# Performance work log

Hardware: AMD Instinct MI355X
Metric: run time of the kernel (lower is better)

## Reference

```python
import jax, jax.numpy as jnp
import numpy as np

B, D, L = 4, 256, 4096

def setup_inputs() -> dict:
    key = jax.random.key(0)
    k1, k2, k3 = jax.random.split(key, 3)
    query = jax.random.normal(k1, (B, D, L), dtype=jnp.float32)
    context = jax.random.normal(k2, (B, D, L), dtype=jnp.float32)
    W_in = jax.random.normal(k3, (D, D), dtype=jnp.float32) * 0.02
    b_in = jnp.zeros((D,), dtype=jnp.float32)
    return {"query": query, "context": context, "W_in": W_in, "b_in": b_in}

def reference(query, context, W_in, b_in):
    # inputs are [B, D, L]; module transposes to [B, L, D]
    q = jnp.transpose(query, (0, 2, 1))    # [B, O, D]
    c = jnp.transpose(context, (0, 2, 1))  # [B, Q, D]
    # 'general': linear_in applied to query only (torch Linear: x @ W^T + b)
    q = q @ W_in.T + b_in
    # unscaled Luong attention: QK^T -> softmax -> A V
    scores = jnp.einsum('bod,bqd->boq', q, c)          # [B, O, Q]
    weights = jax.nn.softmax(scores, axis=-1)          # [B, O, Q]
    out = jnp.einsum('boq,bqd->bod', weights, c)       # [B, O, D]
    return (out, weights)
```

## Files before the change

kernel.cpp:

```cpp
#include <hip/hip_runtime.h>


#define BATCH 4
#define DDIM  256
#define LSEQ  4096
#define TQ    64

typedef float    f32x4 __attribute__((ext_vector_type(4)));
typedef _Float16 f16x8 __attribute__((ext_vector_type(8)));
typedef _Float16 f16x4 __attribute__((ext_vector_type(4)));

__device__ __forceinline__ void gld16(const void* g, void* l) {
  __builtin_amdgcn_global_load_lds((const __attribute__((address_space(1))) void*)g,
                                   (__attribute__((address_space(3))) void*)l, 16, 0, 0);
}

__global__ __launch_bounds__(256) void transpose_cast(
    const float* __restrict__ q_in, const float* __restrict__ c_in,
    _Float16* __restrict__ q_out, _Float16* __restrict__ c_out,
    _Float16* __restrict__ cD16)
{
  __shared__ float tile[64][68];
  const int which = blockIdx.z >> 2;
  const int b     = blockIdx.z & 3;
  const float* __restrict__ src = which ? c_in : q_in;
  _Float16* __restrict__ dst    = which ? c_out : q_out;
  const int l0 = blockIdx.x * 64, d0 = blockIdx.y * 64;
  const int tid = threadIdx.x;
  const int tr = tid >> 4, tc = (tid & 15) << 2;
#pragma unroll
  for (int i = 0; i < 4; ++i) {
    int d = tr + i * 16;
    f32x4 v = *(const f32x4*)(src + ((size_t)b * DDIM + d0 + d) * LSEQ + l0 + tc);
    *(f32x4*)&tile[d][tc] = v;
    if (which) {
      f16x4 h;
      h[0] = (_Float16)v[0]; h[1] = (_Float16)v[1];
      h[2] = (_Float16)v[2]; h[3] = (_Float16)v[3];
      *(f16x4*)(cD16 + ((size_t)b * DDIM + d0 + d) * LSEQ + l0 + tc) = h;
    }
  }
  __syncthreads();
#pragma unroll
  for (int i = 0; i < 4; ++i) {
    int l = tr + i * 16;
    f16x4 h;
    h[0] = (_Float16)tile[tc + 0][l];
    h[1] = (_Float16)tile[tc + 1][l];
    h[2] = (_Float16)tile[tc + 2][l];
    h[3] = (_Float16)tile[tc + 3][l];
    *(f16x4*)(dst + ((size_t)b * LSEQ + l0 + l) * DDIM + d0 + tc) = h;
  }
}

__global__ __launch_bounds__(256) void wconv(const float* __restrict__ w,
                                             _Float16* __restrict__ w16) {
  int i = (blockIdx.x * 256 + threadIdx.x) * 4;
  f32x4 v = *(const f32x4*)(w + i);
  f16x4 h;
  h[0] = (_Float16)v[0]; h[1] = (_Float16)v[1];
  h[2] = (_Float16)v[2]; h[3] = (_Float16)v[3];
  *(f16x4*)(w16 + i) = h;
}

__global__ __launch_bounds__(256) void linear_q(
    const _Float16* __restrict__ qT16, const _Float16* __restrict__ W16,
    const float* __restrict__ bias, _Float16* __restrict__ qw16)
{
  const int tid = threadIdx.x;
  const int wv = tid >> 6, ln = tid & 63, g = ln >> 4, c16 = ln & 15;
  const size_t r0 = (size_t)blockIdx.x * 64 + wv * 16;

  f16x8 qa[8];
  const _Float16* qrow = qT16 + (r0 + c16) * DDIM + g * 8;
#pragma unroll
  for (int kk = 0; kk < 8; ++kk) qa[kk] = *(const f16x8*)(qrow + kk * 32);

  f32x4 acc[16];
#pragma unroll
  for (int n = 0; n < 16; ++n) acc[n] = f32x4{0.f, 0.f, 0.f, 0.f};

#pragma unroll 2
  for (int kk = 0; kk < 8; ++kk) {
#pragma unroll
    for (int n = 0; n < 16; ++n) {
      f16x8 bf = *(const f16x8*)(W16 + (n * 16 + c16) * DDIM + kk * 32 + g * 8);
      acc[n] = __builtin_amdgcn_mfma_f32_16x16x32_f16(qa[kk], bf, acc[n], 0, 0, 0);
    }
  }
#pragma unroll
  for (int n = 0; n < 16; ++n) {
    float bb = bias[n * 16 + c16];
#pragma unroll
    for (int r = 0; r < 4; ++r)
      qw16[(r0 + 4 * g + r) * DDIM + n * 16 + c16] = (_Float16)(acc[n][r] + bb);
  }
}

__global__ __launch_bounds__(1024, 4) void attn_main(
    const _Float16* __restrict__ qw16,
    const _Float16* __restrict__ cT16,
    const _Float16* __restrict__ cD16,
    float* __restrict__ outp,
    float* __restrict__ wgt)
{
  __shared__ __align__(16) char smem[2][32768];
  __shared__ __align__(16) char wbuf[8192];
  __shared__ float redbuf[4][64];
  char* obuf = &smem[0][0];

  const int tid = threadIdx.x;
  const int wv  = tid >> 6;
  const int qw  = wv & 3;
  const int ow  = wv >> 2;
  const int kh  = wv & 1;
  const int dw  = wv >> 1;
  const int ln  = tid & 63;
  const int g   = ln >> 4;
  const int c16 = ln & 15;

  const int lin   = blockIdx.y * 64 + blockIdx.x;
  const int b     = (lin & 7) >> 1;
  const int otile = ((lin >> 3) << 1) | (lin & 1);
  const int o0    = otile * 64;
  const int bo    = b * LSEQ + o0;

  const _Float16* __restrict__ cbase = cT16 + (size_t)b * LSEQ * DDIM;
  const _Float16* __restrict__ cDb   = cD16 + (size_t)b * DDIM * LSEQ;

  f16x8 qb[8];
#pragma unroll
  for (int kk = 0; kk < 8; ++kk)
    qb[kk] = *(const f16x8*)(qw16 +
        ((size_t)(bo + ow * 16 + c16) << 8) + kk * 32 + g * 8);

  auto issue_dma = [&](int t, int pp) {
#pragma unroll
    for (int i = 0; i < 2; ++i) {
      unsigned x  = (unsigned)tid * 16 + i * 16384;
      unsigned q  = x >> 9;
      unsigned db = (x & 511u) ^ ((q & 7u) << 4);
      gld16(cbase + ((size_t)(t * TQ + q) << 8) + (db >> 1), &smem[pp][x]);
    }
  };

  float lsum = 0.f;
  int p = 0;
  issue_dma(0, 0);
  for (int t = 0; t < LSEQ / TQ; ++t) {
    asm volatile("s_waitcnt vmcnt(0)" ::: "memory");
    __builtin_amdgcn_s_barrier();
    issue_dma(t < LSEQ / TQ - 1 ? t + 1 : 0, p ^ 1);
    __builtin_amdgcn_sched_barrier(0);

    const char* cl = smem[p];
    f32x4 sa{0.f, 0.f, 0.f, 0.f};
#pragma unroll
    for (int kk = 0; kk < 8; ++kk) {
      unsigned off = (unsigned)((qw * 16 + c16) * 512 + kk * 64 + g * 16) ^
                     ((unsigned)(c16 & 7) << 4);
      f16x8 af = *(const f16x8*)(cl + off);
      sa = __builtin_amdgcn_mfma_f32_16x16x32_f16(af, qb[kk], sa, 0, 0, 0);
    }
#pragma unroll
    for (int r = 0; r < 4; ++r) lsum += __expf(sa[r]);
    p ^= 1;
  }

  lsum += __shfl_xor(lsum, 16);
  lsum += __shfl_xor(lsum, 32);
  if (ln < 16) redbuf[qw][ow * 16 + ln] = lsum;
  __syncthreads();
  const int o_mine = ow * 16 + c16;
  const float invl = 1.0f / (redbuf[0][o_mine] + redbuf[1][o_mine] +
                             redbuf[2][o_mine] + redbuf[3][o_mine]);

  f32x4 oacc[4][2];
#pragma unroll
  for (int m = 0; m < 4; ++m)
#pragma unroll
    for (int nf = 0; nf < 2; ++nf) oacc[m][nf] = f32x4{0.f, 0.f, 0.f, 0.f};

  for (int t = 0; t < LSEQ / TQ; ++t) {
    const int q0 = t * TQ;
    if (t == 0) asm volatile("s_waitcnt vmcnt(0)" ::: "memory");
    else        asm volatile("s_waitcnt vmcnt(1)" ::: "memory");
    __builtin_amdgcn_s_barrier();
    __builtin_amdgcn_sched_barrier(0);

    f16x8 bv[2];
#pragma unroll
    for (int nf = 0; nf < 2; ++nf)
      bv[nf] = *(const f16x8*)(cDb +
          ((size_t)(dw * 32 + nf * 16 + c16) << 12) + q0 + kh * 32 + g * 8);

    if (t < LSEQ / TQ - 1) issue_dma(t + 1, p ^ 1);

    const char* cl = smem[p];
    f32x4 sa{0.f, 0.f, 0.f, 0.f};
#pragma unroll
    for (int kk = 0; kk < 8; ++kk) {
      unsigned off = (unsigned)((qw * 16 + c16) * 512 + kk * 64 + g * 16) ^
                     ((unsigned)(c16 & 7) << 4);
      f16x8 af = *(const f16x8*)(cl + off);
      sa = __builtin_amdgcn_mfma_f32_16x16x32_f16(af, qb[kk], sa, 0, 0, 0);
    }

    {
      f32x4 wv4;
      f16x4 wh;
#pragma unroll
      for (int r = 0; r < 4; ++r) {
        float w = __expf(sa[r]) * invl;
        wv4[r] = w;
        wh[r]  = (_Float16)w;
      }
      *(f32x4*)(wgt + ((size_t)(bo + o_mine) << 12) + q0 + qw * 16 + 4 * g) = wv4;
      unsigned wb = (unsigned)(o_mine * 128 + (qw * 16 + 4 * g) * 2) ^
                    ((unsigned)(o_mine & 7) << 4);
      *(f16x4*)(wbuf + wb) = wh;
    }
    asm volatile("s_waitcnt lgkmcnt(0)" ::: "memory");
    __builtin_amdgcn_s_barrier();
    __builtin_amdgcn_sched_barrier(0);

#pragma unroll
    for (int m = 0; m < 4; ++m) {
      unsigned off = (unsigned)((m * 16 + c16) * 128 + kh * 64 + g * 16) ^
                     ((unsigned)(c16 & 7) << 4);
      f16x8 wa = *(const f16x8*)(wbuf + off);
#pragma unroll
      for (int nf = 0; nf < 2; ++nf)
        oacc[m][nf] =
            __builtin_amdgcn_mfma_f32_16x16x32_f16(wa, bv[nf], oacc[m][nf], 0, 0, 0);
    }
    p ^= 1;
  }

  __syncthreads();
  if (kh == 1) {
#pragma unroll
    for (int m = 0; m < 4; ++m)
#pragma unroll
      for (int nf = 0; nf < 2; ++nf)
        *(f32x4*)(obuf + dw * 8192 + (m * 2 + nf) * 1024 + ln * 16) = oacc[m][nf];
  }
  __syncthreads();
  if (kh == 0) {
#pragma unroll
    for (int m = 0; m < 4; ++m)
#pragma unroll
      for (int nf = 0; nf < 2; ++nf) {
        f32x4 o2 = *(const f32x4*)(obuf + dw * 8192 + (m * 2 + nf) * 1024 + ln * 16);
        f32x4 o  = oacc[m][nf] + o2;
#pragma unroll
        for (int r = 0; r < 4; ++r)
          outp[((size_t)(bo + m * 16 + 4 * g + r) << 8) + dw * 32 + nf * 16 + c16] = o[r];
      }
  }
}

extern "C" void kernel_launch(void* const* d_in, const int* in_sizes, int n_in,
                              void* d_out, int out_size, void* d_ws, size_t ws_size,
                              hipStream_t stream) {
  const float* query   = (const float*)d_in[0];
  const float* context = (const float*)d_in[1];
  const float* W_in    = (const float*)d_in[2];
  const float* b_in    = (const float*)d_in[3];

  float* outp = (float*)d_out;
  float* wgt  = outp + (size_t)BATCH * LSEQ * DDIM;

  const size_t NELEM = (size_t)BATCH * LSEQ * DDIM;
  _Float16* qT16 = (_Float16*)d_ws;
  _Float16* cT16 = qT16 + NELEM;
  _Float16* qw16 = cT16 + NELEM;
  _Float16* W16  = qw16 + NELEM;
  _Float16* cD16 = W16 + 65536;

  transpose_cast<<<dim3(LSEQ / 64, DDIM / 64, 2 * BATCH), 256, 0, stream>>>(
      query, context, qT16, cT16, cD16);
  wconv<<<(DDIM * DDIM) / 1024, 256, 0, stream>>>(W_in, W16);
  linear_q<<<(BATCH * LSEQ) / 64, 256, 0, stream>>>(qT16, W16, b_in, qw16);
  attn_main<<<dim3(64, BATCH), 1024, 0, stream>>>(qw16, cT16, cD16, outp, wgt);
}
```

Measured before the change: 266.7 us.

## Double query tile per iteration and remap waves to reuse LDS context fragments

Raises the per-iteration context tile from 64 to 128 rows, doubling the LDS double buffers and the weight staging buffer. Each wave now computes scores for two 16-row output fragments against one context fragment, so every LDS read of context feeds two MFMAs, and the barrier count per pass is halved. The cost is 144KB+ of LDS and more registers, which forces one block per CU (launch bounds lowered to 1) and gives less latency hiding across blocks.

```diff
diff --git a/kernel.cpp b/kernel.cpp
--- a/kernel.cpp
+++ b/kernel.cpp
@@ -4,7 +4,7 @@
 #define BATCH 4
 #define DDIM  256
 #define LSEQ  4096
-#define TQ    64
+#define TQ    128
 
 typedef float    f32x4 __attribute__((ext_vector_type(4)));
 typedef _Float16 f16x8 __attribute__((ext_vector_type(8)));
@@ -97,24 +97,24 @@
   }
 }
 
-__global__ __launch_bounds__(1024, 4) void attn_main(
+__global__ __launch_bounds__(1024, 1) void attn_main(
     const _Float16* __restrict__ qw16,
     const _Float16* __restrict__ cT16,
     const _Float16* __restrict__ cD16,
     float* __restrict__ outp,
     float* __restrict__ wgt)
 {
-  __shared__ __align__(16) char smem[2][32768];
-  __shared__ __align__(16) char wbuf[8192];
-  __shared__ float redbuf[4][64];
+  __shared__ __align__(16) char smem[2][65536];
+  __shared__ __align__(16) char wbuf[16384];
+  __shared__ float redbuf[8][64];
   char* obuf = &smem[0][0];
 
   const int tid = threadIdx.x;
   const int wv  = tid >> 6;
-  const int qw  = wv & 3;
-  const int ow  = wv >> 2;
+  const int qs  = wv >> 1;
+  const int os  = wv & 1;
+  const int dw  = wv >> 1;
   const int kh  = wv & 1;
-  const int dw  = wv >> 1;
   const int ln  = tid & 63;
   const int g   = ln >> 4;
   const int c16 = ln & 15;
@@ -128,15 +128,17 @@
   const _Float16* __restrict__ cbase = cT16 + (size_t)b * LSEQ * DDIM;
   const _Float16* __restrict__ cDb   = cD16 + (size_t)b * DDIM * LSEQ;
 
-  f16x8 qb[8];
-#pragma unroll
-  for (int kk = 0; kk < 8; ++kk)
-    qb[kk] = *(const f16x8*)(qw16 +
-        ((size_t)(bo + ow * 16 + c16) << 8) + kk * 32 + g * 8);
+  f16x8 qb[2][8];
+#pragma unroll
+  for (int of = 0; of < 2; ++of)
+#pragma unroll
+    for (int kk = 0; kk < 8; ++kk)
+      qb[of][kk] = *(const f16x8*)(qw16 +
+          ((size_t)(bo + os * 32 + of * 16 + c16) << 8) + kk * 32 + g * 8);
 
   auto issue_dma = [&](int t, int pp) {
 #pragma unroll
-    for (int i = 0; i < 2; ++i) {
+    for (int i = 0; i < 4; ++i) {
       unsigned x  = (unsigned)tid * 16 + i * 16384;
       unsigned q  = x >> 9;
       unsigned db = (x & 511u) ^ ((q & 7u) << 4);
@@ -144,7 +146,20 @@
     }
   };
 
-  float lsum = 0.f;
+  auto scores = [&](const char* cl, f32x4& sa0, f32x4& sa1) {
+    sa0 = f32x4{0.f, 0.f, 0.f, 0.f};
+    sa1 = f32x4{0.f, 0.f, 0.f, 0.f};
+#pragma unroll
+    for (int kk = 0; kk < 8; ++kk) {
+      unsigned off = (unsigned)((qs * 16 + c16) * 512 + kk * 64 + g * 16) ^
+                     ((unsigned)(c16 & 7) << 4);
+      f16x8 af = *(const f16x8*)(cl + off);
+      sa0 = __builtin_amdgcn_mfma_f32_16x16x32_f16(af, qb[0][kk], sa0, 0, 0, 0);
+      sa1 = __builtin_amdgcn_mfma_f32_16x16x32_f16(af, qb[1][kk], sa1, 0, 0, 0);
+    }
+  };
+
+  float lsum0 = 0.f, lsum1 = 0.f;
   int p = 0;
   issue_dma(0, 0);
   for (int t = 0; t < LSEQ / TQ; ++t) {
@@ -153,27 +168,32 @@
     issue_dma(t < LSEQ / TQ - 1 ? t + 1 : 0, p ^ 1);
     __builtin_amdgcn_sched_barrier(0);
 
-    const char* cl = smem[p];
-    f32x4 sa{0.f, 0.f, 0.f, 0.f};
-#pragma unroll
-    for (int kk = 0; kk < 8; ++kk) {
-      unsigned off = (unsigned)((qw * 16 + c16) * 512 + kk * 64 + g * 16) ^
-                     ((unsigned)(c16 & 7) << 4);
-      f16x8 af = *(const f16x8*)(cl + off);
-      sa = __builtin_amdgcn_mfma_f32_16x16x32_f16(af, qb[kk], sa, 0, 0, 0);
-    }
-#pragma unroll
-    for (int r = 0; r < 4; ++r) lsum += __expf(sa[r]);
+    f32x4 sa0, sa1;
+    scores(smem[p], sa0, sa1);
+#pragma unroll
+    for (int r = 0; r < 4; ++r) {
+      lsum0 += __expf(sa0[r]);
+      lsum1 += __expf(sa1[r]);
+    }
     p ^= 1;
   }
 
-  lsum += __shfl_xor(lsum, 16);
-  lsum += __shfl_xor(lsum, 32);
-  if (ln < 16) redbuf[qw][ow * 16 + ln] = lsum;
+  lsum0 += __shfl_xor(lsum0, 16); lsum0 += __shfl_xor(lsum0, 32);
+  lsum1 += __shfl_xor(lsum1, 16); lsum1 += __shfl_xor(lsum1, 32);
+  if (ln < 16) {
+    redbuf[qs][os * 32 + ln]      = lsum0;
+    redbuf[qs][os * 32 + 16 + ln] = lsum1;
+  }
   __syncthreads();
-  const int o_mine = ow * 16 + c16;
-  const float invl = 1.0f / (redbuf[0][o_mine] + redbuf[1][o_mine] +
-                             redbuf[2][o_mine] + redbuf[3][o_mine]);
+  float invl[2];
+#pragma unroll
+  for (int of = 0; of < 2; ++of) {
+    int o = os * 32 + of * 16 + c16;
+    float s = 0.f;
+#pragma unroll
+    for (int k = 0; k < 8; ++k) s += redbuf[k][o];
+    invl[of] = 1.0f / s;
+  }
 
   f32x4 oacc[4][2];
 #pragma unroll
@@ -184,40 +204,39 @@
   for (int t = 0; t < LSEQ / TQ; ++t) {
     const int q0 = t * TQ;
     if (t == 0) asm volatile("s_waitcnt vmcnt(0)" ::: "memory");
-    else        asm volatile("s_waitcnt vmcnt(1)" ::: "memory");
+    else        asm volatile("s_waitcnt vmcnt(2)" ::: "memory");
     __builtin_amdgcn_s_barrier();
     __builtin_amdgcn_sched_barrier(0);
 
-    f16x8 bv[2];
+    f16x8 bv[2][2];
 #pragma unroll
     for (int nf = 0; nf < 2; ++nf)
-      bv[nf] = *(const f16x8*)(cDb +
-          ((size_t)(dw * 32 + nf * 16 + c16) << 12) + q0 + kh * 32 + g * 8);
+#pragma unroll
+      for (int ks = 0; ks < 2; ++ks)
+        bv[nf][ks] = *(const f16x8*)(cDb +
+            ((size_t)(dw * 32 + nf * 16 + c16) << 12) +
+            q0 + kh * 64 + ks * 32 + g * 8);
 
     if (t < LSEQ / TQ - 1) issue_dma(t + 1, p ^ 1);
 
-    const char* cl = smem[p];
-    f32x4 sa{0.f, 0.f, 0.f, 0.f};
-#pragma unroll
-    for (int kk = 0; kk < 8; ++kk) {
-      unsigned off = (unsigned)((qw * 16 + c16) * 512 + kk * 64 + g * 16) ^
-                     ((unsigned)(c16 & 7) << 4);
-      f16x8 af = *(const f16x8*)(cl + off);
-      sa = __builtin_amdgcn_mfma_f32_16x16x32_f16(af, qb[kk], sa, 0, 0, 0);
-    }
-
-    {
+    f32x4 sa0, sa1;
+    scores(smem[p], sa0, sa1);
+
+#pragma unroll
+    for (int of = 0; of < 2; ++of) {
+      f32x4 sv = of ? sa1 : sa0;
       f32x4 wv4;
       f16x4 wh;
 #pragma unroll
       for (int r = 0; r < 4; ++r) {
-        float w = __expf(sa[r]) * invl;
+        float w = __expf(sv[r]) * invl[of];
         wv4[r] = w;
         wh[r]  = (_Float16)w;
       }
-      *(f32x4*)(wgt + ((size_t)(bo + o_mine) << 12) + q0 + qw * 16 + 4 * g) = wv4;
-      unsigned wb = (unsigned)(o_mine * 128 + (qw * 16 + 4 * g) * 2) ^
-                    ((unsigned)(o_mine & 7) << 4);
+      int o = os * 32 + of * 16 + c16;
+      *(f32x4*)(wgt + ((size_t)(bo + o) << 12) + q0 + qs * 16 + 4 * g) = wv4;
+      unsigned wb = (unsigned)(o * 256 + (qs * 16 + 4 * g) * 2) ^
+                    ((unsigned)(o & 7) << 4);
       *(f16x4*)(wbuf + wb) = wh;
     }
     asm volatile("s_waitcnt lgkmcnt(0)" ::: "memory");
@@ -225,14 +244,17 @@
     __builtin_amdgcn_sched_barrier(0);
 
 #pragma unroll
-    for (int m = 0; m < 4; ++m) {
-      unsigned off = (unsigned)((m * 16 + c16) * 128 + kh * 64 + g * 16) ^
-                     ((unsigned)(c16 & 7) << 4);
-      f16x8 wa = *(const f16x8*)(wbuf + off);
-#pragma unroll
-      for (int nf = 0; nf < 2; ++nf)
-        oacc[m][nf] =
-            __builtin_amdgcn_mfma_f32_16x16x32_f16(wa, bv[nf], oacc[m][nf], 0, 0, 0);
+    for (int ks = 0; ks < 2; ++ks) {
+#pragma unroll
+      for (int m = 0; m < 4; ++m) {
+        unsigned off = (unsigned)((m * 16 + c16) * 256 + kh * 128 + ks * 64 + g * 16) ^
+                       ((unsigned)(c16 & 7) << 4);
+        f16x8 wa = *(const f16x8*)(wbuf + off);
+#pragma unroll
+        for (int nf = 0; nf < 2; ++nf)
+          oacc[m][nf] =
+              __builtin_amdgcn_mfma_f32_16x16x32_f16(wa, bv[nf][ks], oacc[m][nf], 0, 0, 0);
+      }
     }
     p ^= 1;
   }
```

Result: slower. 389.0 us (+45.9%).

## Halve attention block to 32 query rows with 512 threads, doubling grid

Applied to the files above, without the earlier changes.

Each attention block now handles 32 query rows with 8 waves instead of 64 rows with 16 waves, and the grid doubles to 512 blocks. Warp roles are remapped so each wave covers 64 output columns with 4 MFMA n-fragments, and context DMA uses 4 loads per thread. Score computation is factored into a lambda and moved ahead of the value loads. This raises block count for better CU load balance, but each block still streams the full context, so total context traffic from L2/LDS doubles.

```diff
diff --git a/kernel.cpp b/kernel.cpp
--- a/kernel.cpp
+++ b/kernel.cpp
@@ -97,7 +97,7 @@
   }
 }
 
-__global__ __launch_bounds__(1024, 4) void attn_main(
+__global__ __launch_bounds__(512, 4) void attn_main(
     const _Float16* __restrict__ qw16,
     const _Float16* __restrict__ cT16,
     const _Float16* __restrict__ cD16,
@@ -105,16 +105,16 @@
     float* __restrict__ wgt)
 {
   __shared__ __align__(16) char smem[2][32768];
-  __shared__ __align__(16) char wbuf[8192];
-  __shared__ float redbuf[4][64];
+  __shared__ __align__(16) char wbuf[4096];
+  __shared__ float redbuf[4][32];
   char* obuf = &smem[0][0];
 
   const int tid = threadIdx.x;
   const int wv  = tid >> 6;
-  const int qw  = wv & 3;
-  const int ow  = wv >> 2;
+  const int qs  = wv >> 1;
+  const int os  = wv & 1;
+  const int dw  = wv >> 1;
   const int kh  = wv & 1;
-  const int dw  = wv >> 1;
   const int ln  = tid & 63;
   const int g   = ln >> 4;
   const int c16 = ln & 15;
@@ -122,7 +122,7 @@
   const int lin   = blockIdx.y * 64 + blockIdx.x;
   const int b     = (lin & 7) >> 1;
   const int otile = ((lin >> 3) << 1) | (lin & 1);
-  const int o0    = otile * 64;
+  const int o0    = otile * 32;
   const int bo    = b * LSEQ + o0;
 
   const _Float16* __restrict__ cbase = cT16 + (size_t)b * LSEQ * DDIM;
@@ -132,19 +132,31 @@
 #pragma unroll
   for (int kk = 0; kk < 8; ++kk)
     qb[kk] = *(const f16x8*)(qw16 +
-        ((size_t)(bo + ow * 16 + c16) << 8) + kk * 32 + g * 8);
+        ((size_t)(bo + os * 16 + c16) << 8) + kk * 32 + g * 8);
 
   auto issue_dma = [&](int t, int pp) {
 #pragma unroll
-    for (int i = 0; i < 2; ++i) {
-      unsigned x  = (unsigned)tid * 16 + i * 16384;
+    for (int i = 0; i < 4; ++i) {
+      unsigned x  = (unsigned)tid * 16 + i * 8192;
       unsigned q  = x >> 9;
       unsigned db = (x & 511u) ^ ((q & 7u) << 4);
       gld16(cbase + ((size_t)(t * TQ + q) << 8) + (db >> 1), &smem[pp][x]);
     }
   };
 
-  float lsum = 0.f;
+  auto scores = [&](const char* cl) {
+    f32x4 sa{0.f, 0.f, 0.f, 0.f};
+#pragma unroll
+    for (int kk = 0; kk < 8; ++kk) {
+      unsigned off = (unsigned)((qs * 16 + c16) * 512 + kk * 64 + g * 16) ^
+                     ((unsigned)(c16 & 7) << 4);
+      f16x8 af = *(const f16x8*)(cl + off);
+      sa = __builtin_amdgcn_mfma_f32_16x16x32_f16(af, qb[kk], sa, 0, 0, 0);
+    }
+    return sa;
+  };
+
+  float ls = 0.f;
   int p = 0;
   issue_dma(0, 0);
   for (int t = 0; t < LSEQ / TQ; ++t) {
@@ -153,33 +165,25 @@
     issue_dma(t < LSEQ / TQ - 1 ? t + 1 : 0, p ^ 1);
     __builtin_amdgcn_sched_barrier(0);
 
-    const char* cl = smem[p];
-    f32x4 sa{0.f, 0.f, 0.f, 0.f};
-#pragma unroll
-    for (int kk = 0; kk < 8; ++kk) {
-      unsigned off = (unsigned)((qw * 16 + c16) * 512 + kk * 64 + g * 16) ^
-                     ((unsigned)(c16 & 7) << 4);
-      f16x8 af = *(const f16x8*)(cl + off);
-      sa = __builtin_amdgcn_mfma_f32_16x16x32_f16(af, qb[kk], sa, 0, 0, 0);
-    }
-#pragma unroll
-    for (int r = 0; r < 4; ++r) lsum += __expf(sa[r]);
+    f32x4 sa = scores(smem[p]);
+#pragma unroll
+    for (int r = 0; r < 4; ++r) ls += __expf(sa[r]);
     p ^= 1;
   }
 
-  lsum += __shfl_xor(lsum, 16);
-  lsum += __shfl_xor(lsum, 32);
-  if (ln < 16) redbuf[qw][ow * 16 + ln] = lsum;
-  __syncthreads();
-  const int o_mine = ow * 16 + c16;
+  ls += __shfl_xor(ls, 16);
+  ls += __shfl_xor(ls, 32);
+  if (ln < 16) redbuf[qs][os * 16 + ln] = ls;
+  __syncthreads();
+  const int o_mine = os * 16 + c16;
   const float invl = 1.0f / (redbuf[0][o_mine] + redbuf[1][o_mine] +
                              redbuf[2][o_mine] + redbuf[3][o_mine]);
 
-  f32x4 oacc[4][2];
-#pragma unroll
-  for (int m = 0; m < 4; ++m)
-#pragma unroll
-    for (int nf = 0; nf < 2; ++nf) oacc[m][nf] = f32x4{0.f, 0.f, 0.f, 0.f};
+  f32x4 oacc[2][4];
+#pragma unroll
+  for (int m = 0; m < 2; ++m)
+#pragma unroll
+    for (int nf = 0; nf < 4; ++nf) oacc[m][nf] = f32x4{0.f, 0.f, 0.f, 0.f};
 
   for (int t = 0; t < LSEQ / TQ; ++t) {
     const int q0 = t * TQ;
@@ -188,23 +192,15 @@
     __builtin_amdgcn_s_barrier();
     __builtin_amdgcn_sched_barrier(0);
 
-    f16x8 bv[2];
-#pragma unroll
-    for (int nf = 0; nf < 2; ++nf)
+    if (t < LSEQ / TQ - 1) issue_dma(t + 1, p ^ 1);
+
+    f32x4 sa = scores(smem[p]);
+
+    f16x8 bv[4];
+#pragma unroll
+    for (int nf = 0; nf < 4; ++nf)
       bv[nf] = *(const f16x8*)(cDb +
-          ((size_t)(dw * 32 + nf * 16 + c16) << 12) + q0 + kh * 32 + g * 8);
-
-    if (t < LSEQ / TQ - 1) issue_dma(t + 1, p ^ 1);
-
-    const char* cl = smem[p];
-    f32x4 sa{0.f, 0.f, 0.f, 0.f};
-#pragma unroll
-    for (int kk = 0; kk < 8; ++kk) {
-      unsigned off = (unsigned)((qw * 16 + c16) * 512 + kk * 64 + g * 16) ^
-                     ((unsigned)(c16 & 7) << 4);
-      f16x8 af = *(const f16x8*)(cl + off);
-      sa = __builtin_amdgcn_mfma_f32_16x16x32_f16(af, qb[kk], sa, 0, 0, 0);
-    }
+          ((size_t)(dw * 64 + nf * 16 + c16) << 12) + q0 + kh * 32 + g * 8);
 
     {
       f32x4 wv4;
@@ -215,8 +211,8 @@
         wv4[r] = w;
         wh[r]  = (_Float16)w;
       }
-      *(f32x4*)(wgt + ((size_t)(bo + o_mine) << 12) + q0 + qw * 16 + 4 * g) = wv4;
-      unsigned wb = (unsigned)(o_mine * 128 + (qw * 16 + 4 * g) * 2) ^
+      *(f32x4*)(wgt + ((size_t)(bo + o_mine) << 12) + q0 + qs * 16 + 4 * g) = wv4;
+      unsigned wb = (unsigned)(o_mine * 128 + (qs * 16 + 4 * g) * 2) ^
                     ((unsigned)(o_mine & 7) << 4);
       *(f16x4*)(wbuf + wb) = wh;
     }
@@ -225,12 +221,12 @@
     __builtin_amdgcn_sched_barrier(0);
 
 #pragma unroll
-    for (int m = 0; m < 4; ++m) {
+    for (int m = 0; m < 2; ++m) {
       unsigned off = (unsigned)((m * 16 + c16) * 128 + kh * 64 + g * 16) ^
                      ((unsigned)(c16 & 7) << 4);
       f16x8 wa = *(const f16x8*)(wbuf + off);
 #pragma unroll
-      for (int nf = 0; nf < 2; ++nf)
+      for (int nf = 0; nf < 4; ++nf)
         oacc[m][nf] =
             __builtin_amdgcn_mfma_f32_16x16x32_f16(wa, bv[nf], oacc[m][nf], 0, 0, 0);
     }
@@ -240,22 +236,22 @@
   __syncthreads();
   if (kh == 1) {
 #pragma unroll
-    for (int m = 0; m < 4; ++m)
-#pragma unroll
-      for (int nf = 0; nf < 2; ++nf)
-        *(f32x4*)(obuf + dw * 8192 + (m * 2 + nf) * 1024 + ln * 16) = oacc[m][nf];
+    for (int m = 0; m < 2; ++m)
+#pragma unroll
+      for (int nf = 0; nf < 4; ++nf)
+        *(f32x4*)(obuf + dw * 8192 + (m * 4 + nf) * 1024 + ln * 16) = oacc[m][nf];
   }
   __syncthreads();
   if (kh == 0) {
 #pragma unroll
-    for (int m = 0; m < 4; ++m)
-#pragma unroll
-      for (int nf = 0; nf < 2; ++nf) {
-        f32x4 o2 = *(const f32x4*)(obuf + dw * 8192 + (m * 2 + nf) * 1024 + ln * 16);
+    for (int m = 0; m < 2; ++m)
+#pragma unroll
+      for (int nf = 0; nf < 4; ++nf) {
+        f32x4 o2 = *(const f32x4*)(obuf + dw * 8192 + (m * 4 + nf) * 1024 + ln * 16);
         f32x4 o  = oacc[m][nf] + o2;
 #pragma unroll
         for (int r = 0; r < 4; ++r)
-          outp[((size_t)(bo + m * 16 + 4 * g + r) << 8) + dw * 32 + nf * 16 + c16] = o[r];
+          outp[((size_t)(bo + m * 16 + 4 * g + r) << 8) + dw * 64 + nf * 16 + c16] = o[r];
       }
   }
 }
@@ -282,5 +278,5 @@
       query, context, qT16, cT16, cD16);
   wconv<<<(DDIM * DDIM) / 1024, 256, 0, stream>>>(W_in, W16);
   linear_q<<<(BATCH * LSEQ) / 64, 256, 0, stream>>>(qT16, W16, b_in, qw16);
-  attn_main<<<dim3(64, BATCH), 1024, 0, stream>>>(qw16, cT16, cD16, outp, wgt);
-}
+  attn_main<<<dim3(64, 8), 512, 0, stream>>>(qw16, cT16, cD16, outp, wgt);
+}
```

Result: slower. 310.7 us (+16.5%).

## Software-pipeline second pass: compute next tile's scores alongside current PV MFMAs

Applied to the files above, without the earlier changes.

Restructures the second pass into a prologue, steady state and epilogue so the QK^T scores for tile t+1 are computed in the same iteration as the weights-times-context MFMAs for tile t. The DMA prefetch now runs two tiles ahead. The exp/normalize/store of the weights happens after a barrier, so the PV and score MFMAs can interleave and one barrier wait per tile is hidden. The risk is higher register pressure and subtle ordering hazards on the shared wbuf and smem buffers.

```diff
diff --git a/kernel.cpp b/kernel.cpp
--- a/kernel.cpp
+++ b/kernel.cpp
@@ -144,7 +144,36 @@
     }
   };
 
-  float lsum = 0.f;
+  auto scores = [&](const char* cl) {
+    f32x4 sa{0.f, 0.f, 0.f, 0.f};
+#pragma unroll
+    for (int kk = 0; kk < 8; ++kk) {
+      unsigned off = (unsigned)((qw * 16 + c16) * 512 + kk * 64 + g * 16) ^
+                     ((unsigned)(c16 & 7) << 4);
+      f16x8 af = *(const f16x8*)(cl + off);
+      sa = __builtin_amdgcn_mfma_f32_16x16x32_f16(af, qb[kk], sa, 0, 0, 0);
+    }
+    return sa;
+  };
+
+  const int o_mine = ow * 16 + c16;
+
+  auto emit_w = [&](const f32x4& sa, int q0, float invl) {
+    f32x4 wv4;
+    f16x4 wh;
+#pragma unroll
+    for (int r = 0; r < 4; ++r) {
+      float w = __expf(sa[r]) * invl;
+      wv4[r] = w;
+      wh[r]  = (_Float16)w;
+    }
+    *(f32x4*)(wgt + ((size_t)(bo + o_mine) << 12) + q0 + qw * 16 + 4 * g) = wv4;
+    unsigned wb = (unsigned)(o_mine * 128 + (qw * 16 + 4 * g) * 2) ^
+                  ((unsigned)(o_mine & 7) << 4);
+    *(f16x4*)(wbuf + wb) = wh;
+  };
+
+  float ls = 0.f;
   int p = 0;
   issue_dma(0, 0);
   for (int t = 0; t < LSEQ / TQ; ++t) {
@@ -153,25 +182,16 @@
     issue_dma(t < LSEQ / TQ - 1 ? t + 1 : 0, p ^ 1);
     __builtin_amdgcn_sched_barrier(0);
 
-    const char* cl = smem[p];
-    f32x4 sa{0.f, 0.f, 0.f, 0.f};
-#pragma unroll
-    for (int kk = 0; kk < 8; ++kk) {
-      unsigned off = (unsigned)((qw * 16 + c16) * 512 + kk * 64 + g * 16) ^
-                     ((unsigned)(c16 & 7) << 4);
-      f16x8 af = *(const f16x8*)(cl + off);
-      sa = __builtin_amdgcn_mfma_f32_16x16x32_f16(af, qb[kk], sa, 0, 0, 0);
-    }
-#pragma unroll
-    for (int r = 0; r < 4; ++r) lsum += __expf(sa[r]);
+    f32x4 sa = scores(smem[p]);
+#pragma unroll
+    for (int r = 0; r < 4; ++r) ls += __expf(sa[r]);
     p ^= 1;
   }
 
-  lsum += __shfl_xor(lsum, 16);
-  lsum += __shfl_xor(lsum, 32);
-  if (ln < 16) redbuf[qw][ow * 16 + ln] = lsum;
+  ls += __shfl_xor(ls, 16);
+  ls += __shfl_xor(ls, 32);
+  if (ln < 16) redbuf[qw][ow * 16 + ln] = ls;
   __syncthreads();
-  const int o_mine = ow * 16 + c16;
   const float invl = 1.0f / (redbuf[0][o_mine] + redbuf[1][o_mine] +
                              redbuf[2][o_mine] + redbuf[3][o_mine]);
 
@@ -181,49 +201,31 @@
 #pragma unroll
     for (int nf = 0; nf < 2; ++nf) oacc[m][nf] = f32x4{0.f, 0.f, 0.f, 0.f};
 
-  for (int t = 0; t < LSEQ / TQ; ++t) {
-    const int q0 = t * TQ;
-    if (t == 0) asm volatile("s_waitcnt vmcnt(0)" ::: "memory");
-    else        asm volatile("s_waitcnt vmcnt(1)" ::: "memory");
+  asm volatile("s_waitcnt vmcnt(0)" ::: "memory");
+  __builtin_amdgcn_s_barrier();
+  issue_dma(1, p ^ 1);
+  __builtin_amdgcn_sched_barrier(0);
+  {
+    f32x4 sa = scores(smem[p]);
+    emit_w(sa, 0, invl);
+  }
+  asm volatile("s_waitcnt lgkmcnt(0)" ::: "memory");
+  __builtin_amdgcn_sched_barrier(0);
+
+  for (int t = 0; t < LSEQ / TQ - 1; ++t) {
+    asm volatile("s_waitcnt vmcnt(1)" ::: "memory");
     __builtin_amdgcn_s_barrier();
     __builtin_amdgcn_sched_barrier(0);
-
+    if (t + 2 <= LSEQ / TQ - 1) issue_dma(t + 2, p);
+
+    const int q0 = t * TQ;
     f16x8 bv[2];
 #pragma unroll
     for (int nf = 0; nf < 2; ++nf)
       bv[nf] = *(const f16x8*)(cDb +
           ((size_t)(dw * 32 + nf * 16 + c16) << 12) + q0 + kh * 32 + g * 8);
 
-    if (t < LSEQ / TQ - 1) issue_dma(t + 1, p ^ 1);
-
-    const char* cl = smem[p];
-    f32x4 sa{0.f, 0.f, 0.f, 0.f};
-#pragma unroll
-    for (int kk = 0; kk < 8; ++kk) {
-      unsigned off = (unsigned)((qw * 16 + c16) * 512 + kk * 64 + g * 16) ^
-                     ((unsigned)(c16 & 7) << 4);
-      f16x8 af = *(const f16x8*)(cl + off);
-      sa = __builtin_amdgcn_mfma_f32_16x16x32_f16(af, qb[kk], sa, 0, 0, 0);
-    }
-
-    {
-      f32x4 wv4;
-      f16x4 wh;
-#pragma unroll
-      for (int r = 0; r < 4; ++r) {
-        float w = __expf(sa[r]) * invl;
-        wv4[r] = w;
-        wh[r]  = (_Float16)w;
-      }
-      *(f32x4*)(wgt + ((size_t)(bo + o_mine) << 12) + q0 + qw * 16 + 4 * g) = wv4;
-      unsigned wb = (unsigned)(o_mine * 128 + (qw * 16 + 4 * g) * 2) ^
-                    ((unsigned)(o_mine & 7) << 4);
-      *(f16x4*)(wbuf + wb) = wh;
-    }
-    asm volatile("s_waitcnt lgkmcnt(0)" ::: "memory");
-    __builtin_amdgcn_s_barrier();
-    __builtin_amdgcn_sched_barrier(0);
-
+    f32x4 sa = scores(smem[p ^ 1]);
 #pragma unroll
     for (int m = 0; m < 4; ++m) {
       unsigned off = (unsigned)((m * 16 + c16) * 128 + kh * 64 + g * 16) ^
@@ -234,7 +236,35 @@
         oacc[m][nf] =
             __builtin_amdgcn_mfma_f32_16x16x32_f16(wa, bv[nf], oacc[m][nf], 0, 0, 0);
     }
+    asm volatile("s_waitcnt lgkmcnt(0)" ::: "memory");
+    __builtin_amdgcn_s_barrier();
+    __builtin_amdgcn_sched_barrier(0);
+
+    emit_w(sa, (t + 1) * TQ, invl);
+    asm volatile("s_waitcnt lgkmcnt(0)" ::: "memory");
+    __builtin_amdgcn_sched_barrier(0);
     p ^= 1;
+  }
+
+  __builtin_amdgcn_s_barrier();
+  __builtin_amdgcn_sched_barrier(0);
+  {
+    const int q0 = (LSEQ / TQ - 1) * TQ;
+    f16x8 bv[2];
+#pragma unroll
+    for (int nf = 0; nf < 2; ++nf)
+      bv[nf] = *(const f16x8*)(cDb +
+          ((size_t)(dw * 32 + nf * 16 + c16) << 12) + q0 + kh * 32 + g * 8);
+#pragma unroll
+    for (int m = 0; m < 4; ++m) {
+      unsigned off = (unsigned)((m * 16 + c16) * 128 + kh * 64 + g * 16) ^
+                     ((unsigned)(c16 & 7) << 4);
+      f16x8 wa = *(const f16x8*)(wbuf + off);
+#pragma unroll
+      for (int nf = 0; nf < 2; ++nf)
+        oacc[m][nf] =
+            __builtin_amdgcn_mfma_f32_16x16x32_f16(wa, bv[nf], oacc[m][nf], 0, 0, 0);
+    }
   }
 
   __syncthreads();
```

Result: slower. 292.6 us (+9.7%).
